# Optimization experiments

Hardware: AMD Instinct MI355X
Metric: run time of the kernel (lower is better)

Reference implementation:

```python
import jax, jax.numpy as jnp
import numpy as np

ROPE_DIM = 64
GN_GROUPS = 8
GN_CH = 512
GN_EPS = 1e-6


def rope_rotate(t, rot_dim=ROPE_DIM, offset=0):
    # lucidrains-style rotary embedding on first rot_dim features, interleaved pairs
    n = t.shape[-2]
    inv_freq = 1.0 / (10000.0 ** (jnp.arange(0, rot_dim, 2, dtype=jnp.float32) / rot_dim))
    pos = jnp.arange(n, dtype=jnp.float32) + offset
    freqs = pos[:, None] * inv_freq[None, :]           # (n, rot_dim//2)
    freqs = jnp.repeat(freqs, 2, axis=-1)              # (n, rot_dim)
    cos, sin = jnp.cos(freqs), jnp.sin(freqs)
    t_rot, t_pass = t[..., :rot_dim], t[..., rot_dim:]
    x = t_rot.reshape(t_rot.shape[:-1] + (rot_dim // 2, 2))
    rot_half = jnp.stack((-x[..., 1], x[..., 0]), axis=-1).reshape(t_rot.shape)
    return jnp.concatenate([t_rot * cos + rot_half * sin, t_pass], axis=-1)


def group_norm_rows(x, w, b, groups=GN_GROUPS, eps=GN_EPS):
    # GroupNorm applied to x reshaped as (-1, C): each row is a sample
    shp = x.shape
    r = x.reshape(-1, groups, GN_CH // groups)
    mu = r.mean(axis=-1, keepdims=True)
    var = r.var(axis=-1, keepdims=True)
    r = (r - mu) * jax.lax.rsqrt(var + eps)
    return (r.reshape(-1, GN_CH) * w + b).reshape(shp)


def setup_inputs() -> dict:
    key = jax.random.key(0)
    ks = jax.random.split(key, 8)
    B, S, D = 4, 8192, 512
    s = 1.0 / np.sqrt(D)
    return {
        "X_Q": jax.random.normal(ks[0], (B, S, D), jnp.float32),
        "X_KV": jax.random.normal(ks[1], (B, S, D), jnp.float32),
        "S_h": jnp.zeros((1,), jnp.float32),
        "S_C": jnp.zeros((1,), jnp.float32),
        "Wq": jax.random.normal(ks[2], (D, D), jnp.float32) * s,
        "bq": jnp.zeros((D,), jnp.float32),
        "Wk": jax.random.normal(ks[3], (D, D), jnp.float32) * s,
        "bk": jnp.zeros((D,), jnp.float32),
        "Wv": jax.random.normal(ks[4], (D, D), jnp.float32) * s,
        "bv": jnp.zeros((D,), jnp.float32),
        "gn_w": jnp.ones((GN_CH,), jnp.float32),
        "gn_b": jnp.zeros((GN_CH,), jnp.float32),
    }


def reference(X_Q, X_KV, S_h, S_C, Wq, bq, Wk, bk, Wv, bv, gn_w, gn_b):
    Q = X_Q @ Wq.T + bq
    V = X_KV @ Wv.T + bv
    # NOTE: faithful to source: K = rope(V), the proj_K output is rotated-V
    _K_unused = X_KV @ Wk.T + bk
    Q = rope_rotate(Q)
    K = rope_rotate(V)
    Q = jax.nn.silu(Q)
    K = jax.nn.silu(K)
    V = jax.nn.silu(V)
    # (Q @ K^T)^T @ V == K @ (Q^T @ V): linear-attention rewrite, O(n*d^2)
    QtV = jnp.einsum('bnd,bne->bde', Q, V)
    out = jnp.einsum('bnd,bde->bne', K, QtV)
    # dropout is identity in eval mode (p=0)
    out = group_norm_rows(out, gn_w, gn_b)
    return (out, S_h, S_C)
```

## Files before the change

kernel.cpp:

```cpp
#include <hip/hip_runtime.h>

typedef __bf16 bf16x8 __attribute__((ext_vector_type(8)));
typedef float f32x4 __attribute__((ext_vector_type(4)));
typedef unsigned short u16x8 __attribute__((ext_vector_type(8)));
typedef unsigned short u16x4 __attribute__((ext_vector_type(4)));

__device__ __forceinline__ unsigned short f2b_u(float f) {
  unsigned int u;
  __builtin_memcpy(&u, &f, 4);
  unsigned int r = 0x7FFFu + ((u >> 16) & 1u);
  return (unsigned short)((u + r) >> 16);
}
__device__ __forceinline__ float silu_f(float x) { return x / (1.f + expf(-x)); }

__global__ __launch_bounds__(256) void cvt_w(const float* __restrict__ in,
                                             unsigned short* __restrict__ out) {
  int i = (blockIdx.x * 256 + threadIdx.x) * 4;
  f32x4 x = *(const f32x4*)(in + i);
  u16x4 o;
#pragma unroll
  for (int j = 0; j < 4; ++j) o[j] = f2b_u(x[j]);
  *(u16x4*)(out + i) = o;
}

__global__ __launch_bounds__(256) void gen_tbl(float* __restrict__ T) {
  int idx = blockIdx.x * 256 + threadIdx.x;
  int pos = idx >> 5, ip = idx & 31;
  float f = (float)pos * powf(10000.f, -(float)ip * (1.f / 32.f));
  float sn, cs;
  sincosf(f, &sn, &cs);
  T[idx * 2] = sn;
  T[idx * 2 + 1] = cs;
}

template <int MODE>
__global__ __launch_bounds__(512, 4) void proj5(
    const float* __restrict__ A, const unsigned short* __restrict__ B,
    unsigned short* __restrict__ Ct, const float* __restrict__ bias,
    unsigned short* __restrict__ Cn, const float* __restrict__ TBL) {
  __shared__ __align__(16) unsigned short sA[64][72];
  __shared__ __align__(16) unsigned short sB[256][72];

  const int bid = blockIdx.x;
  const int n0 = (bid & 1) << 8;
  const long m0 = (long)(bid >> 1) << 6;
  const int tid = threadIdx.x;
  const int lane = tid & 63, w = tid >> 6;
  const int wn = w << 5;
  const int l16 = lane & 15, q8 = (lane >> 4) << 3, rq = (lane >> 4) << 2;
  const int ar = tid >> 3, ac = (tid & 7) << 2;
  const int br = tid >> 1, bc = (tid & 1) << 5;

  const float* Ap = A + (m0 + ar) * 512 + ac;
  const unsigned short* Bp = B + (long)(n0 + br) * 512 + bc;

  f32x4 acc[4][2] = {};
  f32x4 acc2[2][4] = {};

  f32x4 a0 = *(const f32x4*)Ap;
  f32x4 a1 = *(const f32x4*)(Ap + 32);
  u16x8 b0 = *(const u16x8*)Bp;
  u16x8 b1 = *(const u16x8*)(Bp + 8);
  u16x8 b2 = *(const u16x8*)(Bp + 16);
  u16x8 b3 = *(const u16x8*)(Bp + 24);

  for (int kt = 0; kt < 512; kt += 64) {
    __syncthreads();
    {
      u16x4 lo, hi;
#pragma unroll
      for (int j = 0; j < 4; ++j) {
        lo[j] = f2b_u(a0[j]);
        hi[j] = f2b_u(a1[j]);
      }
      *(u16x4*)&sA[ar][ac] = lo;
      *(u16x4*)&sA[ar][ac + 32] = hi;
      *(u16x8*)&sB[br][bc] = b0;
      *(u16x8*)&sB[br][bc + 8] = b1;
      *(u16x8*)&sB[br][bc + 16] = b2;
      *(u16x8*)&sB[br][bc + 24] = b3;
    }
    __syncthreads();
    if (kt < 448) {
      a0 = *(const f32x4*)(Ap + kt + 64);
      a1 = *(const f32x4*)(Ap + kt + 96);
      b0 = *(const u16x8*)(Bp + kt + 64);
      b1 = *(const u16x8*)(Bp + kt + 72);
      b2 = *(const u16x8*)(Bp + kt + 80);
      b3 = *(const u16x8*)(Bp + kt + 88);
    }
#pragma unroll
    for (int kk = 0; kk < 2; ++kk) {
      bf16x8 af[4], bf[2];
#pragma unroll
      for (int i = 0; i < 4; ++i)
        af[i] = *(const bf16x8*)&sA[(i << 4) + l16][(kk << 5) + q8];
#pragma unroll
      for (int j = 0; j < 2; ++j)
        bf[j] = *(const bf16x8*)&sB[wn + (j << 4) + l16][(kk << 5) + q8];
#pragma unroll
      for (int i = 0; i < 4; ++i)
#pragma unroll
        for (int j = 0; j < 2; ++j)
          acc[i][j] = __builtin_amdgcn_mfma_f32_16x16x32_bf16(af[i], bf[j], acc[i][j], 0, 0, 0);
      if (MODE == 1) {
#pragma unroll
        for (int ci = 0; ci < 2; ++ci)
#pragma unroll
          for (int sj = 0; sj < 4; ++sj)
            acc2[ci][sj] =
                __builtin_amdgcn_mfma_f32_16x16x32_bf16(bf[ci], af[sj], acc2[ci][sj], 0, 0, 0);
      }
    }
  }

  const int batch = (int)(m0 >> 13);
  const int s0 = ((int)m0) & 8191;

#pragma unroll
  for (int j = 0; j < 2; ++j) {
    float bv = bias[n0 + wn + (j << 4) + l16];
#pragma unroll
    for (int i = 0; i < 4; ++i)
#pragma unroll
      for (int r = 0; r < 4; ++r) acc[i][j][r] += bv;
  }

  if (MODE == 0) {
    if (n0 + wn < 64) {
#pragma unroll
      for (int j = 0; j < 2; ++j) {
        int ip = ((wn + (j << 4)) >> 1) + (l16 >> 1);
        float sgn = (l16 & 1) ? 1.f : -1.f;
#pragma unroll
        for (int i = 0; i < 4; ++i)
#pragma unroll
          for (int r = 0; r < 4; ++r) {
            int pos = s0 + (i << 4) + rq + r;
            const float* t = TBL + ((long)pos << 6) + (ip << 1);
            float sn = t[0], cs = t[1];
            float v = acc[i][j][r];
            float p = __shfl_xor(v, 1);
            acc[i][j][r] = v * cs + sgn * sn * p;
          }
      }
    }
  }

  {
    unsigned short* dstT = Ct + ((long)batch << 22);
#pragma unroll
    for (int i = 0; i < 4; ++i)
#pragma unroll
      for (int j = 0; j < 2; ++j) {
        u16x4 o;
#pragma unroll
        for (int r = 0; r < 4; ++r) o[r] = f2b_u(silu_f(acc[i][j][r]));
        *(u16x4*)(dstT + (long)(n0 + wn + (j << 4) + l16) * 8192 + s0 + (i << 4) + rq) = o;
      }
  }

  if (MODE == 1) {
#pragma unroll
    for (int ci = 0; ci < 2; ++ci) {
      float bv2[4];
#pragma unroll
      for (int r = 0; r < 4; ++r) bv2[r] = bias[n0 + wn + (ci << 4) + rq + r];
#pragma unroll
      for (int sj = 0; sj < 4; ++sj)
#pragma unroll
        for (int r = 0; r < 4; ++r) acc2[ci][sj][r] += bv2[r];
    }
    if (n0 + wn < 64) {
#pragma unroll
      for (int ci = 0; ci < 2; ++ci)
#pragma unroll
        for (int sj = 0; sj < 4; ++sj) {
          int pos = s0 + (sj << 4) + l16;
          const float* tb = TBL + ((long)pos << 6);
#pragma unroll
          for (int rp = 0; rp < 4; rp += 2) {
            int ip = (wn + (ci << 4) + rq + rp) >> 1;
            float sn = tb[ip << 1], cs = tb[(ip << 1) + 1];
            float v0 = acc2[ci][sj][rp], v1 = acc2[ci][sj][rp + 1];
            acc2[ci][sj][rp] = v0 * cs - sn * v1;
            acc2[ci][sj][rp + 1] = v1 * cs + sn * v0;
          }
        }
    }
    unsigned short* dstN = Cn + ((long)batch << 22);
#pragma unroll
    for (int ci = 0; ci < 2; ++ci)
#pragma unroll
      for (int sj = 0; sj < 4; ++sj) {
        u16x4 o;
#pragma unroll
        for (int r = 0; r < 4; ++r) o[r] = f2b_u(silu_f(acc2[ci][sj][r]));
        int seq = s0 + (sj << 4) + l16;
        *(u16x4*)(dstN + (long)seq * 512 + n0 + wn + (ci << 4) + rq) = o;
      }
  }
}

__global__ __launch_bounds__(256) void gemm_qtv(
    const unsigned short* __restrict__ A, const unsigned short* __restrict__ B,
    float* __restrict__ Cp) {
  __shared__ __align__(16) unsigned short smem[18432];
  unsigned short(*sA)[72] = (unsigned short(*)[72])smem;
  unsigned short(*sB)[72] = (unsigned short(*)[72])(smem + 9216);

  const int blk = blockIdx.x;
  const int low3 = blk & 7, hi = blk >> 3;
  const int m = ((low3 & 1) << 1) | (hi & 1);
  const int n = (low3 & 2) | ((hi >> 1) & 1);
  const int z = ((hi >> 2) << 1) | (low3 >> 2);
  const int batch = z >> 3, kc = z & 7;
  const unsigned short* A0 = A + (long)batch * 4194304 + (long)kc * 1024;
  const unsigned short* B0 = B + (long)batch * 4194304 + (long)kc * 1024;
  const int m0 = m << 7, n0 = n << 7;
  const int tid = threadIdx.x;
  const int lane = tid & 63, wave = tid >> 6;
  const int wm = (wave & 1) << 6, wn = (wave >> 1) << 6;
  const int l16 = lane & 15, q8 = (lane >> 4) << 3;

  f32x4 acc[4][4] = {};

  for (int kt = 0; kt < 1024; kt += 64) {
    u16x8 ra[4], rb[4];
#pragma unroll
    for (int i = 0; i < 4; ++i) {
      int c = tid + (i << 8);
      int row = c >> 3, col = (c & 7) << 3;
      ra[i] = *(const u16x8*)(A0 + (long)(m0 + row) * 8192 + kt + col);
      rb[i] = *(const u16x8*)(B0 + (long)(n0 + row) * 8192 + kt + col);
    }
    __syncthreads();
#pragma unroll
    for (int i = 0; i < 4; ++i) {
      int c = tid + (i << 8);
      int row = c >> 3, col = (c & 7) << 3;
      *(u16x8*)&sA[row][col] = ra[i];
      *(u16x8*)&sB[row][col] = rb[i];
    }
    __syncthreads();
#pragma unroll
    for (int kk = 0; kk < 2; ++kk) {
      bf16x8 af[4], bfv[4];
#pragma unroll
      for (int i = 0; i < 4; ++i) {
        af[i] = *(const bf16x8*)&sA[wm + (i << 4) + l16][(kk << 5) + q8];
        bfv[i] = *(const bf16x8*)&sB[wn + (i << 4) + l16][(kk << 5) + q8];
      }
#pragma unroll
      for (int i = 0; i < 4; ++i)
#pragma unroll
        for (int j = 0; j < 4; ++j)
          acc[i][j] = __builtin_amdgcn_mfma_f32_16x16x32_bf16(af[i], bfv[j], acc[i][j], 0, 0, 0);
    }
  }

  const int rq = (lane >> 4) << 2;
#pragma unroll
  for (int i = 0; i < 4; ++i)
#pragma unroll
    for (int j = 0; j < 4; ++j)
#pragma unroll
      for (int r = 0; r < 4; ++r) {
        int gm = m0 + wm + (i << 4) + rq + r;
        int gn = n0 + wn + (j << 4) + l16;
        atomicAdd(Cp + (long)batch * 262144 + (long)gm * 512 + gn, acc[i][j][r]);
      }
}

__global__ __launch_bounds__(64) void colmean(const float* __restrict__ C, float* __restrict__ Cd) {
  const int bd = blockIdx.x;
  const int b = bd >> 9, d = bd & 511;
  const float* p = C + ((long)b << 18) + d;
  float s = 0.f;
  for (int e = threadIdx.x; e < 512; e += 64) s += p[(long)e << 9];
  s += __shfl_xor(s, 1);
  s += __shfl_xor(s, 2);
  s += __shfl_xor(s, 4);
  s += __shfl_xor(s, 8);
  s += __shfl_xor(s, 16);
  s += __shfl_xor(s, 32);
  if (threadIdx.x == 0) Cd[bd] = s * (1.f / 512.f);
}

__global__ __launch_bounds__(256) void cvt_center(const float* __restrict__ in,
                                                  const float* __restrict__ Cd,
                                                  unsigned short* __restrict__ out,
                                                  const float* __restrict__ Sh,
                                                  const float* __restrict__ Sc,
                                                  float* __restrict__ outp) {
  int i = (blockIdx.x * 256 + threadIdx.x) * 4;
  f32x4 x = *(const f32x4*)(in + i);
  int b = i >> 18, d = i & 511;
  f32x4 c = *(const f32x4*)(Cd + (b << 9) + d);
  u16x4 o;
#pragma unroll
  for (int j = 0; j < 4; ++j) o[j] = f2b_u(x[j] - c[j]);
  *(u16x4*)(out + i) = o;
  if (blockIdx.x == 0 && threadIdx.x == 0) {
    outp[16777216] = Sh[0];
    outp[16777217] = Sc[0];
  }
}

__global__ __launch_bounds__(256) void gemm4_gn(
    const unsigned short* __restrict__ A, const unsigned short* __restrict__ B,
    const float* __restrict__ gnw, const float* __restrict__ gnb,
    float* __restrict__ out) {
  __shared__ __align__(16) unsigned short smem[18432];
  unsigned short(*sA)[72] = (unsigned short(*)[72])smem;
  unsigned short(*sB)[72] = (unsigned short(*)[72])(smem + 9216);

  const int blk = blockIdx.x;
  const int mt = blk & 255, n = blk >> 8;
  const int batch = mt >> 6;
  const int m0 = (mt & 63) << 7, n0 = n << 7;
  const unsigned short* A0 = A + (long)batch * 4194304;
  const unsigned short* B0 = B + (long)batch * 262144;
  const int tid = threadIdx.x;
  const int lane = tid & 63, wave = tid >> 6;
  const int wm = (wave & 1) << 6, wn = (wave >> 1) << 6;
  const int l16 = lane & 15, q8 = (lane >> 4) << 3;

  f32x4 acc[4][4] = {};

  for (int kt = 0; kt < 512; kt += 64) {
    u16x8 ra[4], rb[4];
#pragma unroll
    for (int i = 0; i < 4; ++i) {
      int c = tid + (i << 8);
      int row = c >> 3, col = (c & 7) << 3;
      ra[i] = *(const u16x8*)(A0 + (long)(m0 + row) * 512 + kt + col);
      rb[i] = *(const u16x8*)(B0 + (long)(n0 + row) * 512 + kt + col);
    }
    __syncthreads();
#pragma unroll
    for (int i = 0; i < 4; ++i) {
      int c = tid + (i << 8);
      int row = c >> 3, col = (c & 7) << 3;
      *(u16x8*)&sA[row][col] = ra[i];
      *(u16x8*)&sB[row][col] = rb[i];
    }
    __syncthreads();
#pragma unroll
    for (int kk = 0; kk < 2; ++kk) {
      bf16x8 af[4], bfv[4];
#pragma unroll
      for (int i = 0; i < 4; ++i) {
        af[i] = *(const bf16x8*)&sA[wm + (i << 4) + l16][(kk << 5) + q8];
        bfv[i] = *(const bf16x8*)&sB[wn + (i << 4) + l16][(kk << 5) + q8];
      }
#pragma unroll
      for (int i = 0; i < 4; ++i)
#pragma unroll
        for (int j = 0; j < 4; ++j)
          acc[i][j] = __builtin_amdgcn_mfma_f32_16x16x32_bf16(af[i], bfv[j], acc[i][j], 0, 0, 0);
    }
  }

  const int rq = (lane >> 4) << 2;
  float wv[4], bb[4];
#pragma unroll
  for (int j = 0; j < 4; ++j) {
    int gn = n0 + wn + (j << 4) + l16;
    wv[j] = gnw[gn];
    bb[j] = gnb[gn];
  }
  float* obase = out + (long)batch * 4194304;
#pragma unroll
  for (int i = 0; i < 4; ++i) {
    float mean[4], inv[4];
#pragma unroll
    for (int r = 0; r < 4; ++r) {
      float s = acc[i][0][r] + acc[i][1][r] + acc[i][2][r] + acc[i][3][r];
      s += __shfl_xor(s, 1);
      s += __shfl_xor(s, 2);
      s += __shfl_xor(s, 4);
      s += __shfl_xor(s, 8);
      mean[r] = s * (1.f / 64.f);
      float sq = 0.f;
#pragma unroll
      for (int j = 0; j < 4; ++j) {
        float d = acc[i][j][r] - mean[r];
        sq += d * d;
      }
      sq += __shfl_xor(sq, 1);
      sq += __shfl_xor(sq, 2);
      sq += __shfl_xor(sq, 4);
      sq += __shfl_xor(sq, 8);
      inv[r] = rsqrtf(sq * (1.f / 64.f) + 1e-6f);
    }
#pragma unroll
    for (int j = 0; j < 4; ++j) {
      int gn = n0 + wn + (j << 4) + l16;
#pragma unroll
      for (int r = 0; r < 4; ++r) {
        int gm = m0 + wm + (i << 4) + rq + r;
        obase[(long)gm * 512 + gn] = (acc[i][j][r] - mean[r]) * inv[r] * wv[j] + bb[j];
      }
    }
  }
}

extern "C" void kernel_launch(void* const* d_in, const int* in_sizes, int n_in,
                              void* d_out, int out_size, void* d_ws, size_t ws_size,
                              hipStream_t stream) {
  const float* Xq = (const float*)d_in[0];
  const float* Xkv = (const float*)d_in[1];
  const float* Sh = (const float*)d_in[2];
  const float* Sc = (const float*)d_in[3];
  const float* Wq = (const float*)d_in[4];
  const float* bq = (const float*)d_in[5];
  const float* Wv = (const float*)d_in[8];
  const float* bv = (const float*)d_in[9];
  const float* gnw = (const float*)d_in[10];
  const float* gnb = (const float*)d_in[11];

  char* ws = (char*)d_ws;
  unsigned short* QT = (unsigned short*)(ws);
  unsigned short* VT = (unsigned short*)(ws + 33554432L);
  unsigned short* Kn = (unsigned short*)(ws + 67108864L);
  float* C2f = (float*)(ws + 100663296L);
  unsigned short* C2c = (unsigned short*)(ws + 104857600L);
  float* Cd = (float*)(ws + 106954752L);
  unsigned short* Wqb = (unsigned short*)(ws + 100663296L);
  unsigned short* Wvb = (unsigned short*)(ws + 100663296L + 524288L);
  float* TBL = (float*)(ws + 100663296L + 1048576L);
  float* outp = (float*)d_out;

  if (ws_size < 106962944UL) return;

  cvt_w<<<256, 256, 0, stream>>>(Wq, Wqb);
  cvt_w<<<256, 256, 0, stream>>>(Wv, Wvb);
  gen_tbl<<<1024, 256, 0, stream>>>(TBL);

  proj5<0><<<1024, 512, 0, stream>>>(Xq, Wqb, QT, bq, nullptr, TBL);
  proj5<1><<<1024, 512, 0, stream>>>(Xkv, Wvb, VT, bv, Kn, TBL);

  (void)hipMemsetAsync(C2f, 0, 4194304, stream);
  gemm_qtv<<<512, 256, 0, stream>>>(VT, QT, C2f);

  colmean<<<2048, 64, 0, stream>>>(C2f, Cd);
  cvt_center<<<1024, 256, 0, stream>>>(C2f, Cd, C2c, Sh, Sc, outp);

  gemm4_gn<<<1024, 256, 0, stream>>>(Kn, C2c, gnw, gnb, outp);
}
```

Measured before the change: 360.8 us.

## Merge setup and projection launches, prefetch GEMM tiles, replace atomics with partial reduce

Merges the weight-conversion and rope-table kernels into one launch, and merges the Q and V projection templates into a single grid that picks its mode from the block index. Both GEMM kernels now prefetch the next K-tile into registers while computing on the current one. The split-K atomicAdd, along with its memset, is replaced by plain stores of partial sums into scratch space in the output buffer, followed by a separate 8-way reduction kernel. This trades fewer launches, no atomics and better load overlap for higher register pressure and extra memory traffic on the partials.

```diff
diff --git a/kernel.cpp b/kernel.cpp
--- a/kernel.cpp
+++ b/kernel.cpp
@@ -13,37 +13,50 @@
 }
 __device__ __forceinline__ float silu_f(float x) { return x / (1.f + expf(-x)); }
 
-__global__ __launch_bounds__(256) void cvt_w(const float* __restrict__ in,
-                                             unsigned short* __restrict__ out) {
-  int i = (blockIdx.x * 256 + threadIdx.x) * 4;
-  f32x4 x = *(const f32x4*)(in + i);
-  u16x4 o;
-#pragma unroll
-  for (int j = 0; j < 4; ++j) o[j] = f2b_u(x[j]);
-  *(u16x4*)(out + i) = o;
-}
-
-__global__ __launch_bounds__(256) void gen_tbl(float* __restrict__ T) {
-  int idx = blockIdx.x * 256 + threadIdx.x;
-  int pos = idx >> 5, ip = idx & 31;
-  float f = (float)pos * powf(10000.f, -(float)ip * (1.f / 32.f));
-  float sn, cs;
-  sincosf(f, &sn, &cs);
-  T[idx * 2] = sn;
-  T[idx * 2 + 1] = cs;
-}
-
-template <int MODE>
-__global__ __launch_bounds__(512, 4) void proj5(
-    const float* __restrict__ A, const unsigned short* __restrict__ B,
-    unsigned short* __restrict__ Ct, const float* __restrict__ bias,
-    unsigned short* __restrict__ Cn, const float* __restrict__ TBL) {
+__global__ __launch_bounds__(256) void setup_k(const float* __restrict__ Wq,
+                                               const float* __restrict__ Wv,
+                                               unsigned short* __restrict__ Wqb,
+                                               unsigned short* __restrict__ Wvb,
+                                               float* __restrict__ T) {
+  int b = blockIdx.x;
+  if (b < 512) {
+    const float* in = (b < 256) ? Wq : Wv;
+    unsigned short* out = (b < 256) ? Wqb : Wvb;
+    int i = ((b & 255) * 256 + threadIdx.x) * 4;
+    f32x4 x = *(const f32x4*)(in + i);
+    u16x4 o;
+#pragma unroll
+    for (int j = 0; j < 4; ++j) o[j] = f2b_u(x[j]);
+    *(u16x4*)(out + i) = o;
+  } else {
+    int idx = (b - 512) * 256 + threadIdx.x;
+    int pos = idx >> 5, ip = idx & 31;
+    float f = (float)pos * powf(10000.f, -(float)ip * (1.f / 32.f));
+    float sn, cs;
+    sincosf(f, &sn, &cs);
+    T[idx * 2] = sn;
+    T[idx * 2 + 1] = cs;
+  }
+}
+
+__global__ __launch_bounds__(512, 4) void proj6(
+    const float* __restrict__ Xq, const float* __restrict__ Xkv,
+    const unsigned short* __restrict__ Wqb, const unsigned short* __restrict__ Wvb,
+    const float* __restrict__ bq, const float* __restrict__ bv,
+    unsigned short* __restrict__ QT, unsigned short* __restrict__ VT,
+    unsigned short* __restrict__ Kn, const float* __restrict__ TBL) {
   __shared__ __align__(16) unsigned short sA[64][72];
   __shared__ __align__(16) unsigned short sB[256][72];
 
-  const int bid = blockIdx.x;
-  const int n0 = (bid & 1) << 8;
-  const long m0 = (long)(bid >> 1) << 6;
+  const int mode = blockIdx.x & 1;
+  const int t = blockIdx.x >> 1;
+  const float* A = mode ? Xkv : Xq;
+  const unsigned short* B = mode ? Wvb : Wqb;
+  const float* bias = mode ? bv : bq;
+  unsigned short* Ct = mode ? VT : QT;
+
+  const int n0 = (t & 1) << 8;
+  const long m0 = (long)(t >> 1) << 6;
   const int tid = threadIdx.x;
   const int lane = tid & 63, w = tid >> 6;
   const int wn = w << 5;
@@ -93,17 +106,15 @@
     for (int kk = 0; kk < 2; ++kk) {
       bf16x8 af[4], bf[2];
 #pragma unroll
-      for (int i = 0; i < 4; ++i)
-        af[i] = *(const bf16x8*)&sA[(i << 4) + l16][(kk << 5) + q8];
-#pragma unroll
-      for (int j = 0; j < 2; ++j)
-        bf[j] = *(const bf16x8*)&sB[wn + (j << 4) + l16][(kk << 5) + q8];
+      for (int i = 0; i < 4; ++i) af[i] = *(const bf16x8*)&sA[(i << 4) + l16][(kk << 5) + q8];
+#pragma unroll
+      for (int j = 0; j < 2; ++j) bf[j] = *(const bf16x8*)&sB[wn + (j << 4) + l16][(kk << 5) + q8];
 #pragma unroll
       for (int i = 0; i < 4; ++i)
 #pragma unroll
         for (int j = 0; j < 2; ++j)
           acc[i][j] = __builtin_amdgcn_mfma_f32_16x16x32_bf16(af[i], bf[j], acc[i][j], 0, 0, 0);
-      if (MODE == 1) {
+      if (mode == 1) {
 #pragma unroll
         for (int ci = 0; ci < 2; ++ci)
 #pragma unroll
@@ -119,14 +130,14 @@
 
 #pragma unroll
   for (int j = 0; j < 2; ++j) {
-    float bv = bias[n0 + wn + (j << 4) + l16];
+    float bv_ = bias[n0 + wn + (j << 4) + l16];
 #pragma unroll
     for (int i = 0; i < 4; ++i)
 #pragma unroll
-      for (int r = 0; r < 4; ++r) acc[i][j][r] += bv;
-  }
-
-  if (MODE == 0) {
+      for (int r = 0; r < 4; ++r) acc[i][j][r] += bv_;
+  }
+
+  if (mode == 0) {
     if (n0 + wn < 64) {
 #pragma unroll
       for (int j = 0; j < 2; ++j) {
@@ -137,8 +148,8 @@
 #pragma unroll
           for (int r = 0; r < 4; ++r) {
             int pos = s0 + (i << 4) + rq + r;
-            const float* t = TBL + ((long)pos << 6) + (ip << 1);
-            float sn = t[0], cs = t[1];
+            const float* tb = TBL + ((long)pos << 6) + (ip << 1);
+            float sn = tb[0], cs = tb[1];
             float v = acc[i][j][r];
             float p = __shfl_xor(v, 1);
             acc[i][j][r] = v * cs + sgn * sn * p;
@@ -160,7 +171,7 @@
       }
   }
 
-  if (MODE == 1) {
+  if (mode == 1) {
 #pragma unroll
     for (int ci = 0; ci < 2; ++ci) {
       float bv2[4];
@@ -188,7 +199,7 @@
           }
         }
     }
-    unsigned short* dstN = Cn + ((long)batch << 22);
+    unsigned short* dstN = Kn + ((long)batch << 22);
 #pragma unroll
     for (int ci = 0; ci < 2; ++ci)
 #pragma unroll
@@ -204,7 +215,7 @@
 
 __global__ __launch_bounds__(256) void gemm_qtv(
     const unsigned short* __restrict__ A, const unsigned short* __restrict__ B,
-    float* __restrict__ Cp) {
+    float* __restrict__ P) {
   __shared__ __align__(16) unsigned short smem[18432];
   unsigned short(*sA)[72] = (unsigned short(*)[72])smem;
   unsigned short(*sB)[72] = (unsigned short(*)[72])(smem + 9216);
@@ -225,15 +236,16 @@
 
   f32x4 acc[4][4] = {};
 
+  u16x8 ra[4], rb[4];
+#pragma unroll
+  for (int i = 0; i < 4; ++i) {
+    int c = tid + (i << 8);
+    int row = c >> 3, col = (c & 7) << 3;
+    ra[i] = *(const u16x8*)(A0 + (long)(m0 + row) * 8192 + col);
+    rb[i] = *(const u16x8*)(B0 + (long)(n0 + row) * 8192 + col);
+  }
+
   for (int kt = 0; kt < 1024; kt += 64) {
-    u16x8 ra[4], rb[4];
-#pragma unroll
-    for (int i = 0; i < 4; ++i) {
-      int c = tid + (i << 8);
-      int row = c >> 3, col = (c & 7) << 3;
-      ra[i] = *(const u16x8*)(A0 + (long)(m0 + row) * 8192 + kt + col);
-      rb[i] = *(const u16x8*)(B0 + (long)(n0 + row) * 8192 + kt + col);
-    }
     __syncthreads();
 #pragma unroll
     for (int i = 0; i < 4; ++i) {
@@ -243,6 +255,15 @@
       *(u16x8*)&sB[row][col] = rb[i];
     }
     __syncthreads();
+    if (kt < 960) {
+#pragma unroll
+      for (int i = 0; i < 4; ++i) {
+        int c = tid + (i << 8);
+        int row = c >> 3, col = (c & 7) << 3;
+        ra[i] = *(const u16x8*)(A0 + (long)(m0 + row) * 8192 + kt + 64 + col);
+        rb[i] = *(const u16x8*)(B0 + (long)(n0 + row) * 8192 + kt + 64 + col);
+      }
+    }
 #pragma unroll
     for (int kk = 0; kk < 2; ++kk) {
       bf16x8 af[4], bfv[4];
@@ -260,6 +281,7 @@
   }
 
   const int rq = (lane >> 4) << 2;
+  float* P0 = P + ((long)z << 18);
 #pragma unroll
   for (int i = 0; i < 4; ++i)
 #pragma unroll
@@ -268,8 +290,22 @@
       for (int r = 0; r < 4; ++r) {
         int gm = m0 + wm + (i << 4) + rq + r;
         int gn = n0 + wn + (j << 4) + l16;
-        atomicAdd(Cp + (long)batch * 262144 + (long)gm * 512 + gn, acc[i][j][r]);
-      }
+        P0[(long)gm * 512 + gn] = acc[i][j][r];
+      }
+}
+
+__global__ __launch_bounds__(256) void reduce8(const float* __restrict__ P,
+                                               float* __restrict__ C2f) {
+  int i = (blockIdx.x * 256 + threadIdx.x) * 4;
+  int b = i >> 18, off = i & 262143;
+  const float* p = P + ((long)(b << 3) << 18) + off;
+  f32x4 s = *(const f32x4*)p;
+#pragma unroll
+  for (int kc = 1; kc < 8; ++kc) {
+    f32x4 v = *(const f32x4*)(p + ((long)kc << 18));
+    s += v;
+  }
+  *(f32x4*)(C2f + i) = s;
 }
 
 __global__ __launch_bounds__(64) void colmean(const float* __restrict__ C, float* __restrict__ Cd) {
@@ -328,15 +364,16 @@
 
   f32x4 acc[4][4] = {};
 
+  u16x8 ra[4], rb[4];
+#pragma unroll
+  for (int i = 0; i < 4; ++i) {
+    int c = tid + (i << 8);
+    int row = c >> 3, col = (c & 7) << 3;
+    ra[i] = *(const u16x8*)(A0 + (long)(m0 + row) * 512 + col);
+    rb[i] = *(const u16x8*)(B0 + (long)(n0 + row) * 512 + col);
+  }
+
   for (int kt = 0; kt < 512; kt += 64) {
-    u16x8 ra[4], rb[4];
-#pragma unroll
-    for (int i = 0; i < 4; ++i) {
-      int c = tid + (i << 8);
-      int row = c >> 3, col = (c & 7) << 3;
-      ra[i] = *(const u16x8*)(A0 + (long)(m0 + row) * 512 + kt + col);
-      rb[i] = *(const u16x8*)(B0 + (long)(n0 + row) * 512 + kt + col);
-    }
     __syncthreads();
 #pragma unroll
     for (int i = 0; i < 4; ++i) {
@@ -346,6 +383,15 @@
       *(u16x8*)&sB[row][col] = rb[i];
     }
     __syncthreads();
+    if (kt < 448) {
+#pragma unroll
+      for (int i = 0; i < 4; ++i) {
+        int c = tid + (i << 8);
+        int row = c >> 3, col = (c & 7) << 3;
+        ra[i] = *(const u16x8*)(A0 + (long)(m0 + row) * 512 + kt + 64 + col);
+        rb[i] = *(const u16x8*)(B0 + (long)(n0 + row) * 512 + kt + 64 + col);
+      }
+    }
 #pragma unroll
     for (int kk = 0; kk < 2; ++kk) {
       bf16x8 af[4], bfv[4];
@@ -431,18 +477,17 @@
   unsigned short* Wvb = (unsigned short*)(ws + 100663296L + 524288L);
   float* TBL = (float*)(ws + 100663296L + 1048576L);
   float* outp = (float*)d_out;
+  float* Pp = (float*)d_out;
 
   if (ws_size < 106962944UL) return;
 
-  cvt_w<<<256, 256, 0, stream>>>(Wq, Wqb);
-  cvt_w<<<256, 256, 0, stream>>>(Wv, Wvb);
-  gen_tbl<<<1024, 256, 0, stream>>>(TBL);
-
-  proj5<0><<<1024, 512, 0, stream>>>(Xq, Wqb, QT, bq, nullptr, TBL);
-  proj5<1><<<1024, 512, 0, stream>>>(Xkv, Wvb, VT, bv, Kn, TBL);
-
-  (void)hipMemsetAsync(C2f, 0, 4194304, stream);
-  gemm_qtv<<<512, 256, 0, stream>>>(VT, QT, C2f);
+  setup_k<<<1536, 256, 0, stream>>>(Wq, Wv, Wqb, Wvb, TBL);
+
+  proj6<<<2048, 512, 0, stream>>>(Xq, Xkv, Wqb, Wvb, bq, bv, QT, VT, Kn, TBL);
+
+  gemm_qtv<<<512, 256, 0, stream>>>(VT, QT, Pp);
+
+  reduce8<<<1024, 256, 0, stream>>>(Pp, C2f);
 
   colmean<<<2048, 64, 0, stream>>>(C2f, Cd);
   cvt_center<<<1024, 256, 0, stream>>>(C2f, Cd, C2c, Sh, Sc, outp);
```

After: 346.1 us. 4.1% less time.
